# Optimization experiments

Measured on AMD Instinct MI355X. Metric: run time of the kernel, lower is better.

Reference implementation:

```python
import jax, jax.numpy as jnp
import numpy as np
from jax import lax

TEMP = 0.1  # softmax_temp default in forward


def _conv(x, w, b):
    y = lax.conv_general_dilated(x, w, (1, 1), 'VALID',
                                 dimension_numbers=('NCHW', 'OIHW', 'NCHW'))
    return y + b[None, :, None, None]


def _avg_pool2(x):
    # AvgPool2d(2,2), floor mode (VALID window)
    s = lax.reduce_window(x, 0.0, lax.add, (1, 1, 2, 2), (1, 1, 2, 2), 'VALID')
    return s / 4.0


def _cnn(x, c1w, c1b, c2w, c2b, c3w, c3b, dw, db):
    x = _avg_pool2(jax.nn.relu(_conv(x, c1w, c1b)))   # (N,8,13,13)
    x = _avg_pool2(jax.nn.relu(_conv(x, c2w, c2b)))   # (N,16,5,5)
    x = _avg_pool2(jax.nn.relu(_conv(x, c3w, c3b)))   # (N,32,1,1)
    x = x.reshape(x.shape[0], -1)                      # (N,32)
    logits = x @ dw.T + db                             # (N,10)
    return jax.nn.softmax(logits, axis=1)


def _digit_to_rule(p):
    # p: (N,10) -> (N,6)
    return jnp.stack([p[:, 8], p[:, 4] + p[:, 6], p[:, 0] + p[:, 2],
                      p[:, 7] + p[:, 9], p[:, 5], p[:, 1] + p[:, 3]], axis=1)


def setup_inputs() -> dict:
    key = jax.random.key(0)
    ks = jax.random.split(key, 10)
    B, T, D, C, H, W = 256, 8, 4, 1, 28, 28
    sc = 0.1
    return {
        'sequences': jax.random.normal(ks[0], (B, T, D, C, H, W), jnp.float32),
        'conv1_w': jax.random.normal(ks[1], (8, 1, 3, 3), jnp.float32) * sc,
        'conv1_b': jax.random.normal(ks[2], (8,), jnp.float32) * sc,
        'conv2_w': jax.random.normal(ks[3], (16, 8, 3, 3), jnp.float32) * sc,
        'conv2_b': jax.random.normal(ks[4], (16,), jnp.float32) * sc,
        'conv3_w': jax.random.normal(ks[5], (32, 16, 3, 3), jnp.float32) * sc,
        'conv3_b': jax.random.normal(ks[6], (32,), jnp.float32) * sc,
        'dense_w': jax.random.normal(ks[7], (10, 32), jnp.float32) * sc,
        'dense_b': jax.random.normal(ks[8], (10,), jnp.float32) * sc,
        'trans': jax.nn.softmax(jax.random.normal(ks[9], (6, 9, 10), jnp.float32), axis=-1),
    }


def reference(sequences, conv1_w, conv1_b, conv2_w, conv2_b, conv3_w, conv3_b,
              dense_w, dense_b, trans):
    B, T, D, C, H, W = sequences.shape
    S = trans.shape[2]           # num_states = 10
    N = T * D                    # number of recurrence steps
    # CNN is independent per (t,d,b): batch all images at once.
    imgs = jnp.transpose(sequences, (1, 2, 0, 3, 4, 5)).reshape(N * B, C, H, W)
    digit_probs = _cnn(imgs, conv1_w, conv1_b, conv2_w, conv2_b,
                       conv3_w, conv3_b, dense_w, dense_b)      # (N*B,10)
    guard_probs = _digit_to_rule(digit_probs)                   # (N*B,6)

    # Per-rule transition matrices: softmax with temperature + fixed accepting row.
    M = jax.nn.softmax(trans / TEMP, axis=-1)                   # (R,S-1,S)
    acc = jnp.zeros((S,), M.dtype).at[-1].set(1.0)
    M = jnp.concatenate([M, jnp.broadcast_to(acc, (M.shape[0], 1, S))], axis=1)  # (R,S,S)

    # Effective transition matrices per step and batch element.
    g = guard_probs.reshape(N, B, -1)
    A_all = jnp.einsum('nbr,rij->nbij', g, M)                   # (N,B,S,S)

    state0 = jnp.zeros((B, S), sequences.dtype).at[:, 0].set(1.0)

    def step(state, A):
        return jnp.einsum('bi,bij->bj', state, A), None

    state_final, _ = lax.scan(step, state0, A_all)
    all_cnn_preds = digit_probs.reshape(N, B, -1)
    all_guard_preds = g
    return all_cnn_preds, all_guard_preds, state_final
```

## Files before the change

### kernel.cpp

```cpp
#include <hip/hip_runtime.h>

typedef _Float16 half_t;
typedef _Float16 h2 __attribute__((ext_vector_type(2)));
typedef _Float16 h4 __attribute__((ext_vector_type(4)));

__device__ __forceinline__ float fdot2f(h2 a, h2 b, float c) {
#if __has_builtin(__builtin_amdgcn_fdot2)
    return __builtin_amdgcn_fdot2(a, b, c, false);
#else
    return c + (float)a.x * (float)b.x + (float)a.y * (float)b.y;
#endif
}

__global__ __launch_bounds__(256) void prep_kernel(
    const float* __restrict__ w2g, const float* __restrict__ w3g,
    const float* __restrict__ wdg, float* __restrict__ wsW)
{
    const int tid = threadIdx.x;
    half_t* w2h = (half_t*)(wsW + 320);
    half_t* w3h = w2h + 1152;
    for (int i = tid; i < 320; i += 256) {
        int j = i >> 5, c2 = i & 31;
        wsW[c2 * 10 + j] = wdg[i];
    }
    for (int i = tid; i < 1152; i += 256) {
        int l = i & 3, c = (i >> 2) & 15, g = (i >> 6) & 1, k = i >> 7;
        w2h[i] = (half_t)w2g[(c * 8 + g * 4 + l) * 9 + k];
    }
    for (int i = tid; i < 4608; i += 256) {
        int l = i & 3, c = (i >> 2) & 31, g = (i >> 7) & 3, k = i >> 9;
        w3h[i] = (half_t)w3g[(c * 16 + g * 4 + l) * 9 + k];
    }
}

__global__ __launch_bounds__(256) void cnn_kernel(
    const float* __restrict__ seq,
    const float* __restrict__ w1g, const float* __restrict__ b1g,
    const float* __restrict__ b2g, const float* __restrict__ b3g,
    const float* __restrict__ bdg, const float* __restrict__ wsW,
    float* __restrict__ out, float* __restrict__ g_ws)
{
    __shared__ __align__(16) half_t s_img2[4][28][28];
    __shared__ __align__(16) half_t s_p1n[4][2][10][11][4];
    __shared__ __align__(16) half_t s_p2n[4][16][16];
    __shared__ float s_c3[4][32][4];
    __shared__ float s_p3[4][32];
    __shared__ float s_logit[4][10];
    __shared__ float s_prob[4][10];

    const int tid   = threadIdx.x;
    const int mbase = blockIdx.x * 4;
    const float*  wdt = wsW;
    const half_t* w2h = (const half_t*)(wsW + 320);
    const half_t* w3h = w2h + 1152;

    if (tid < 196) {
        #pragma unroll
        for (int img = 0; img < 4; img++) {
            const int m = mbase + img;
            const int b = m & 255, nn = m >> 8;
            const int t = nn >> 2, dd = nn & 3;
            const float4* s4 = (const float4*)(seq + (((size_t)b * 8 + t) * 4 + dd) * 784);
            float4 v = s4[tid];
            int flat = tid * 4;
            int r  = flat / 28;
            int cb = flat - r * 28;
            int e  = cb >> 1;
            h2 ev = { (half_t)v.x, (half_t)v.z };
            h2 od = { (half_t)v.y, (half_t)v.w };
            *(h2*)&s_img2[img][r][e]      = ev;
            *(h2*)&s_img2[img][r][14 + e] = od;
        }
    }
    __syncthreads();

    for (int idx = tid; idx < 400; idx += 256) {
        const int img = idx / 100;
        const int rem = idx - img * 100;
        const int y   = rem / 10;
        const int x   = rem - y * 10;
        const int r0  = 2 * y;
        float p[4][4];
        #pragma unroll
        for (int i = 0; i < 4; i++) {
            const half_t* rp = &s_img2[img][r0 + i][0];
            p[i][0] = (float)rp[x];
            p[i][1] = (float)rp[14 + x];
            p[i][2] = (float)rp[x + 1];
            p[i][3] = (float)rp[15 + x];
        }
        float res[8];
        #pragma unroll
        for (int c = 0; c < 8; c++) {
            float w[9];
            #pragma unroll
            for (int k = 0; k < 9; k++) w[k] = w1g[c * 9 + k];
            const float bias = b1g[c];
            float acc = 0.f;
            #pragma unroll
            for (int rr = 0; rr < 2; rr++)
                #pragma unroll
                for (int cc = 0; cc < 2; cc++) {
                    float v = bias;
                    #pragma unroll
                    for (int i = 0; i < 3; i++)
                        #pragma unroll
                        for (int j = 0; j < 3; j++)
                            v += p[rr + i][cc + j] * w[i * 3 + j];
                    acc += fmaxf(v, 0.f);
                }
            res[c] = 0.25f * acc;
        }
        const int slot = (x >> 1) + 5 * (x & 1);
        h4 lo = { (half_t)res[0], (half_t)res[1], (half_t)res[2], (half_t)res[3] };
        h4 hi = { (half_t)res[4], (half_t)res[5], (half_t)res[6], (half_t)res[7] };
        *(h4*)&s_p1n[img][0][y][slot][0] = lo;
        *(h4*)&s_p1n[img][1][y][slot][0] = hi;
    }
    __syncthreads();

    const int img2 = tid >> 6;
    const int t6   = tid & 63;

    {
        const int pos = t6 >> 2;
        const int q   = t6 & 3;
        const int y   = pos >> 2, x = pos & 3;
        const int r0  = 2 * y;
        const int slotm[4] = { x, 5 + x, x + 1, 6 + x };
        float v[4][4];
        #pragma unroll
        for (int oc = 0; oc < 4; oc++) {
            const float bias = b2g[q * 4 + oc];
            #pragma unroll
            for (int w2 = 0; w2 < 4; w2++) v[oc][w2] = bias;
        }
        #pragma unroll
        for (int g = 0; g < 2; g++) {
            h2 aL[4][4], aH[4][4];
            #pragma unroll
            for (int i = 0; i < 4; i++)
                #pragma unroll
                for (int dx = 0; dx < 4; dx++) {
                    h4 a = *(const h4*)&s_p1n[img2][g][r0 + i][slotm[dx]][0];
                    aL[i][dx] = __builtin_shufflevector(a, a, 0, 1);
                    aH[i][dx] = __builtin_shufflevector(a, a, 2, 3);
                }
            #pragma unroll
            for (int k = 0; k < 9; k++) {
                const int di = k / 3, dj = k - di * 3;
                #pragma unroll
                for (int oc = 0; oc < 4; oc++) {
                    h4 w = *(const h4*)&w2h[((k * 2 + g) * 16 + q * 4 + oc) * 4];
                    h2 wL = __builtin_shufflevector(w, w, 0, 1);
                    h2 wH = __builtin_shufflevector(w, w, 2, 3);
                    #pragma unroll
                    for (int rr = 0; rr < 2; rr++)
                        #pragma unroll
                        for (int cc = 0; cc < 2; cc++) {
                            float* acc = &v[oc][rr * 2 + cc];
                            *acc = fdot2f(aL[rr + di][cc + dj], wL, *acc);
                            *acc = fdot2f(aH[rr + di][cc + dj], wH, *acc);
                        }
                }
            }
        }
        float res[4];
        #pragma unroll
        for (int oc = 0; oc < 4; oc++)
            res[oc] = 0.25f * (fmaxf(v[oc][0], 0.f) + fmaxf(v[oc][1], 0.f) +
                               fmaxf(v[oc][2], 0.f) + fmaxf(v[oc][3], 0.f));
        h4 o = { (half_t)res[0], (half_t)res[1], (half_t)res[2], (half_t)res[3] };
        *(h4*)&s_p2n[img2][pos][q * 4] = o;
    }
    __syncthreads();

    {
        const int c = t6 >> 1;
        const int u = t6 & 1;
        float acc0 = b3g[c], acc1 = acc0;
        #pragma unroll
        for (int g = 0; g < 4; g++) {
            h2 AL[3][4], AH[3][4];
            #pragma unroll
            for (int i = 0; i < 3; i++)
                #pragma unroll
                for (int jj = 0; jj < 4; jj++) {
                    h4 a = *(const h4*)&s_p2n[img2][(u + i) * 4 + jj][g * 4];
                    AL[i][jj] = __builtin_shufflevector(a, a, 0, 1);
                    AH[i][jj] = __builtin_shufflevector(a, a, 2, 3);
                }
            #pragma unroll
            for (int i = 0; i < 3; i++)
                #pragma unroll
                for (int j = 0; j < 3; j++) {
                    const int k = i * 3 + j;
                    h4 w = *(const h4*)&w3h[((k * 4 + g) * 32 + c) * 4];
                    h2 wL = __builtin_shufflevector(w, w, 0, 1);
                    h2 wH = __builtin_shufflevector(w, w, 2, 3);
                    acc0 = fdot2f(AL[i][j], wL, acc0);
                    acc0 = fdot2f(AH[i][j], wH, acc0);
                    acc1 = fdot2f(AL[i][j + 1], wL, acc1);
                    acc1 = fdot2f(AH[i][j + 1], wH, acc1);
                }
        }
        s_c3[img2][c][u * 2 + 0] = fmaxf(acc0, 0.f);
        s_c3[img2][c][u * 2 + 1] = fmaxf(acc1, 0.f);
    }
    __syncthreads();
    if (t6 < 32)
        s_p3[img2][t6] = 0.25f * (s_c3[img2][t6][0] + s_c3[img2][t6][1] +
                                  s_c3[img2][t6][2] + s_c3[img2][t6][3]);
    __syncthreads();

    if (t6 < 10) {
        float acc = bdg[t6];
        #pragma unroll
        for (int c2 = 0; c2 < 32; c2++) acc += s_p3[img2][c2] * wdt[c2 * 10 + t6];
        s_logit[img2][t6] = acc;
    }
    __syncthreads();
    if (t6 < 10) {
        const int m = mbase + img2;
        float mx = s_logit[img2][0];
        #pragma unroll
        for (int k = 1; k < 10; k++) mx = fmaxf(mx, s_logit[img2][k]);
        float ssum = 0.f;
        #pragma unroll
        for (int k = 0; k < 10; k++) ssum += __expf(s_logit[img2][k] - mx);
        float p = __expf(s_logit[img2][t6] - mx) / ssum;
        s_prob[img2][t6] = p;
        out[(size_t)m * 10 + t6] = p;
    }
    __syncthreads();
    if (t6 < 6) {
        const int m = mbase + img2;
        int ia = (0x157048 >> (t6 * 4)) & 0xF;
        int ib = (0x3F926F >> (t6 * 4)) & 0xF;
        float gv = s_prob[img2][ia] + (ib < 10 ? s_prob[img2][ib] : 0.f);
        out[81920 + (size_t)m * 6 + t6] = gv;
        g_ws[(size_t)m * 6 + t6] = gv;
    }
}

__global__ __launch_bounds__(256) void sfa_kernel(
    const float* __restrict__ trans,
    const float* __restrict__ g_ws,
    float* __restrict__ out)
{
    __shared__ float M[600];
    const int tid  = threadIdx.x;
    const int lane = tid & 63;
    const int wv   = tid >> 6;

    if (tid < 54) {
        int r = tid / 9, i = tid - r * 9;
        const float* row = trans + (size_t)(r * 9 + i) * 10;
        float x[10], mx = -1e30f;
        #pragma unroll
        for (int j = 0; j < 10; j++) { x[j] = 10.f * row[j]; mx = fmaxf(mx, x[j]); }
        float s = 0.f;
        #pragma unroll
        for (int j = 0; j < 10; j++) { x[j] = __expf(x[j] - mx); s += x[j]; }
        float inv = 1.f / s;
        #pragma unroll
        for (int j = 0; j < 10; j++) M[(r * 9 + i) * 10 + j] = x[j] * inv;
    }
    __syncthreads();

    const int bb    = lane / 10;
    const int j     = lane - bb * 10;
    const int base  = bb * 10;
    const bool ok   = (bb < 6);
    int batch = blockIdx.x * 24 + wv * 6 + bb;
    const bool live = ok && (batch < 256);
    if (!live) batch = 0;

    float Mreg[54];
    #pragma unroll
    for (int k = 0; k < 54; k++) Mreg[k] = M[k * 10 + j];

    float stj = (j == 0) ? 1.f : 0.f;

    for (int nn = 0; nn < 32; nn++) {
        const float* gp = g_ws + ((size_t)nn * 256 + batch) * 6;
        float2 ga = *(const float2*)(gp);
        float2 gb = *(const float2*)(gp + 2);
        float2 gc = *(const float2*)(gp + 4);
        float g[6] = {ga.x, ga.y, gb.x, gb.y, gc.x, gc.y};

        float st[10];
        #pragma unroll
        for (int i = 0; i < 10; i++) st[i] = __shfl(stj, base + i, 64);

        float gsum = g[0] + g[1] + g[2] + g[3] + g[4] + g[5];
        float ns = (j == 9) ? gsum * st[9] : 0.f;
        #pragma unroll
        for (int r = 0; r < 6; r++) {
            float h = 0.f;
            #pragma unroll
            for (int i = 0; i < 9; i++) h += st[i] * Mreg[r * 9 + i];
            ns += g[r] * h;
        }
        stj = ns;
    }
    if (live) out[131072 + (size_t)batch * 10 + j] = stj;
}

extern "C" void kernel_launch(void* const* d_in, const int* in_sizes, int n_in,
                              void* d_out, int out_size, void* d_ws, size_t ws_size,
                              hipStream_t stream) {
    const float* seq = (const float*)d_in[0];
    const float* w1  = (const float*)d_in[1];
    const float* b1  = (const float*)d_in[2];
    const float* w2  = (const float*)d_in[3];
    const float* b2  = (const float*)d_in[4];
    const float* w3  = (const float*)d_in[5];
    const float* b3  = (const float*)d_in[6];
    const float* wd  = (const float*)d_in[7];
    const float* bd  = (const float*)d_in[8];
    const float* tr  = (const float*)d_in[9];
    float* out  = (float*)d_out;
    float* g_ws = (float*)d_ws;
    float* wsW  = g_ws + 49152;

    prep_kernel<<<1, 256, 0, stream>>>(w2, w3, wd, wsW);
    cnn_kernel<<<2048, 256, 0, stream>>>(seq, w1, b1, b2, b3, bd, wsW, out, g_ws);
    sfa_kernel<<<11, 256, 0, stream>>>(tr, g_ws, out);
}
```

Baseline: 148.7 us.

## Replace CNN tail shared-memory reductions with wave shuffles and retune the conv kernel

The conv3 pooling, dense softmax and guard mapping now use wave shuffles (__shfl_xor / __shfl) instead of shared-memory staging, which removes several __syncthreads barriers and the s_c3/s_logit/s_prob buffers. The input image is staged in LDS as fp32 instead of fp16, dropping the conversions at the cost of more shared memory. conv2/conv3 weights are preloaded into registers per output channel before the dot loops. A minimum-blocks hint of 6 is added to launch_bounds to cap register use. The register preloads and the occupancy cap can pull against each other and may cause spills.

```diff
diff --git a/kernel.cpp b/kernel.cpp
--- a/kernel.cpp
+++ b/kernel.cpp
@@ -33,20 +33,17 @@
     }
 }
 
-__global__ __launch_bounds__(256) void cnn_kernel(
+__global__ __launch_bounds__(256, 6) void cnn_kernel(
     const float* __restrict__ seq,
     const float* __restrict__ w1g, const float* __restrict__ b1g,
     const float* __restrict__ b2g, const float* __restrict__ b3g,
     const float* __restrict__ bdg, const float* __restrict__ wsW,
     float* __restrict__ out, float* __restrict__ g_ws)
 {
-    __shared__ __align__(16) half_t s_img2[4][28][28];
+    __shared__ __align__(16) float  s_img2[4][28][28];
     __shared__ __align__(16) half_t s_p1n[4][2][10][11][4];
     __shared__ __align__(16) half_t s_p2n[4][16][16];
-    __shared__ float s_c3[4][32][4];
     __shared__ float s_p3[4][32];
-    __shared__ float s_logit[4][10];
-    __shared__ float s_prob[4][10];
 
     const int tid   = threadIdx.x;
     const int mbase = blockIdx.x * 4;
@@ -66,10 +63,8 @@
             int r  = flat / 28;
             int cb = flat - r * 28;
             int e  = cb >> 1;
-            h2 ev = { (half_t)v.x, (half_t)v.z };
-            h2 od = { (half_t)v.y, (half_t)v.w };
-            *(h2*)&s_img2[img][r][e]      = ev;
-            *(h2*)&s_img2[img][r][14 + e] = od;
+            *(float2*)&s_img2[img][r][e]      = make_float2(v.x, v.z);
+            *(float2*)&s_img2[img][r][14 + e] = make_float2(v.y, v.w);
         }
     }
     __syncthreads();
@@ -83,11 +78,11 @@
         float p[4][4];
         #pragma unroll
         for (int i = 0; i < 4; i++) {
-            const half_t* rp = &s_img2[img][r0 + i][0];
-            p[i][0] = (float)rp[x];
-            p[i][1] = (float)rp[14 + x];
-            p[i][2] = (float)rp[x + 1];
-            p[i][3] = (float)rp[15 + x];
+            const float* rp = &s_img2[img][r0 + i][0];
+            p[i][0] = rp[x];
+            p[i][1] = rp[14 + x];
+            p[i][2] = rp[x + 1];
+            p[i][3] = rp[15 + x];
         }
         float res[8];
         #pragma unroll
@@ -147,13 +142,16 @@
                     aH[i][dx] = __builtin_shufflevector(a, a, 2, 3);
                 }
             #pragma unroll
-            for (int k = 0; k < 9; k++) {
-                const int di = k / 3, dj = k - di * 3;
-                #pragma unroll
-                for (int oc = 0; oc < 4; oc++) {
-                    h4 w = *(const h4*)&w2h[((k * 2 + g) * 16 + q * 4 + oc) * 4];
-                    h2 wL = __builtin_shufflevector(w, w, 0, 1);
-                    h2 wH = __builtin_shufflevector(w, w, 2, 3);
+            for (int oc = 0; oc < 4; oc++) {
+                h4 wk[9];
+                #pragma unroll
+                for (int k = 0; k < 9; k++)
+                    wk[k] = *(const h4*)&w2h[((k * 2 + g) * 16 + q * 4 + oc) * 4];
+                #pragma unroll
+                for (int k = 0; k < 9; k++) {
+                    const int di = k / 3, dj = k - di * 3;
+                    h2 wL = __builtin_shufflevector(wk[k], wk[k], 0, 1);
+                    h2 wH = __builtin_shufflevector(wk[k], wk[k], 2, 3);
                     #pragma unroll
                     for (int rr = 0; rr < 2; rr++)
                         #pragma unroll
@@ -190,56 +188,56 @@
                     AL[i][jj] = __builtin_shufflevector(a, a, 0, 1);
                     AH[i][jj] = __builtin_shufflevector(a, a, 2, 3);
                 }
-            #pragma unroll
-            for (int i = 0; i < 3; i++)
-                #pragma unroll
-                for (int j = 0; j < 3; j++) {
-                    const int k = i * 3 + j;
-                    h4 w = *(const h4*)&w3h[((k * 4 + g) * 32 + c) * 4];
-                    h2 wL = __builtin_shufflevector(w, w, 0, 1);
-                    h2 wH = __builtin_shufflevector(w, w, 2, 3);
-                    acc0 = fdot2f(AL[i][j], wL, acc0);
-                    acc0 = fdot2f(AH[i][j], wH, acc0);
-                    acc1 = fdot2f(AL[i][j + 1], wL, acc1);
-                    acc1 = fdot2f(AH[i][j + 1], wH, acc1);
-                }
-        }
-        s_c3[img2][c][u * 2 + 0] = fmaxf(acc0, 0.f);
-        s_c3[img2][c][u * 2 + 1] = fmaxf(acc1, 0.f);
-    }
-    __syncthreads();
-    if (t6 < 32)
-        s_p3[img2][t6] = 0.25f * (s_c3[img2][t6][0] + s_c3[img2][t6][1] +
-                                  s_c3[img2][t6][2] + s_c3[img2][t6][3]);
-    __syncthreads();
-
-    if (t6 < 10) {
-        float acc = bdg[t6];
-        #pragma unroll
-        for (int c2 = 0; c2 < 32; c2++) acc += s_p3[img2][c2] * wdt[c2 * 10 + t6];
-        s_logit[img2][t6] = acc;
-    }
-    __syncthreads();
-    if (t6 < 10) {
+            h4 wk[9];
+            #pragma unroll
+            for (int k = 0; k < 9; k++)
+                wk[k] = *(const h4*)&w3h[((k * 4 + g) * 32 + c) * 4];
+            #pragma unroll
+            for (int k = 0; k < 9; k++) {
+                const int i = k / 3, j = k - i * 3;
+                h2 wL = __builtin_shufflevector(wk[k], wk[k], 0, 1);
+                h2 wH = __builtin_shufflevector(wk[k], wk[k], 2, 3);
+                acc0 = fdot2f(AL[i][j], wL, acc0);
+                acc0 = fdot2f(AH[i][j], wH, acc0);
+                acc1 = fdot2f(AL[i][j + 1], wL, acc1);
+                acc1 = fdot2f(AH[i][j + 1], wH, acc1);
+            }
+        }
+        float s = fmaxf(acc0, 0.f) + fmaxf(acc1, 0.f);
+        s += __shfl_xor(s, 1, 64);
+        if (u == 0) s_p3[img2][c] = 0.25f * s;
+    }
+    __syncthreads();
+
+    {
+        float logit = -1e30f;
+        if (t6 < 10) {
+            float acc = bdg[t6];
+            #pragma unroll
+            for (int c2 = 0; c2 < 32; c2++) acc += s_p3[img2][c2] * wdt[c2 * 10 + t6];
+            logit = acc;
+        }
+        float mx = logit;
+        #pragma unroll
+        for (int s = 1; s < 16; s <<= 1) mx = fmaxf(mx, __shfl_xor(mx, s, 16));
+        float e = (t6 < 10) ? __expf(logit - mx) : 0.f;
+        float ssum = e;
+        #pragma unroll
+        for (int s = 1; s < 16; s <<= 1) ssum += __shfl_xor(ssum, s, 16);
+        float p = e / ssum;
         const int m = mbase + img2;
-        float mx = s_logit[img2][0];
-        #pragma unroll
-        for (int k = 1; k < 10; k++) mx = fmaxf(mx, s_logit[img2][k]);
-        float ssum = 0.f;
-        #pragma unroll
-        for (int k = 0; k < 10; k++) ssum += __expf(s_logit[img2][k] - mx);
-        float p = __expf(s_logit[img2][t6] - mx) / ssum;
-        s_prob[img2][t6] = p;
-        out[(size_t)m * 10 + t6] = p;
-    }
-    __syncthreads();
-    if (t6 < 6) {
-        const int m = mbase + img2;
-        int ia = (0x157048 >> (t6 * 4)) & 0xF;
-        int ib = (0x3F926F >> (t6 * 4)) & 0xF;
-        float gv = s_prob[img2][ia] + (ib < 10 ? s_prob[img2][ib] : 0.f);
-        out[81920 + (size_t)m * 6 + t6] = gv;
-        g_ws[(size_t)m * 6 + t6] = gv;
+        if (t6 < 10) out[(size_t)m * 10 + t6] = p;
+
+        const int sh = (t6 < 6 ? t6 : 0) * 4;
+        const int ia = (0x157048 >> sh) & 0xF;
+        const int ib = (0x3F926F >> sh) & 0xF;
+        float pa = __shfl(p, ia, 16);
+        float pb = __shfl(p, ib, 16);
+        if (t6 < 6) {
+            float gv = pa + pb;
+            out[81920 + (size_t)m * 6 + t6] = gv;
+            g_ws[(size_t)m * 6 + t6] = gv;
+        }
     }
 }
 
```

Result: faster. 138.6 us (-6.8%).
